# Kernel optimization log

Measured on AMD Instinct MI355X. Metric: run time of the kernel, lower is better.

## Reference

```python
import jax, jax.numpy as jnp
import numpy as np

N = 50000      # nodes
E = 800000     # edges
F = 500        # num_features
HID = 64       # hidden_channels
H = 4          # num_heads
HC = HID // H  # headc = 16
C = 8          # num_classes
KHOP = 2       # K hops
CST = 1e-5


def setup_inputs() -> dict:
    key = jax.random.key(0)
    ks = jax.random.split(key, 12)
    s = 0.02
    return {
        "node_feat": jax.random.normal(ks[0], (N, F), dtype=jnp.float32),
        "edge_index": jax.random.randint(ks[1], (2, E), 0, N, dtype=jnp.int64),
        "Wi": jax.random.normal(ks[2], (F, HID), dtype=jnp.float32) * s,
        "bi": jnp.zeros((HID,), dtype=jnp.float32),
        "Wq": jax.random.normal(ks[3], (HID, H * HC), dtype=jnp.float32) * s,
        "bq": jnp.zeros((H * HC,), dtype=jnp.float32),
        "Wk": jax.random.normal(ks[4], (HID, H * HC), dtype=jnp.float32) * s,
        "bk": jnp.zeros((H * HC,), dtype=jnp.float32),
        "Wv": jax.random.normal(ks[5], (HID, H * C), dtype=jnp.float32) * s,
        "bv": jnp.zeros((H * C,), dtype=jnp.float32),
        "Wo": jax.random.normal(ks[6], (H * C, C), dtype=jnp.float32) * s,
        "bo": jnp.zeros((C,), dtype=jnp.float32),
        "hopwise": jnp.ones((KHOP + 1,), dtype=jnp.float32),
        "headwise": jnp.zeros((H, KHOP), dtype=jnp.float32),
        "teleport": jnp.ones((1,), dtype=jnp.float32),
    }


def reference(node_feat, edge_index, Wi, bi, Wq, bq, Wk, bk, Wv, bv, Wo, bo,
              hopwise, headwise, teleport):
    row, col = edge_index[0], edge_index[1]
    # degree(col): in-degree; norm = deg^-1 indexed at row (as in the torch code)
    deg = jax.ops.segment_sum(jnp.ones((E,), dtype=node_feat.dtype), col,
                              num_segments=N)
    deg_inv = jnp.where(deg > 0, 1.0 / deg, 0.0)  # [N]

    x = jax.nn.relu(node_feat @ Wi + bi)          # dropout p=0.0 / eval -> identity
    Q = (1.0 + jax.nn.elu(x @ Wq + bq)).reshape(N, H, HC)
    Kf = (1.0 + jax.nn.elu(x @ Wk + bk)).reshape(N, H, HC)
    V = (x @ Wv + bv).reshape(N, H, C)

    M = jnp.einsum('nhi,nhj->nhij', Kf, V)        # [N,H,HC,C]
    hidden = V * hopwise[0]                       # ind_gamma & gamma_softmax
    layerwise = jax.nn.softmax(headwise, axis=0)  # softmax over heads (dim=-2)

    # global attention (teleport) term
    teleportM = jnp.sum(M, axis=0, keepdims=True) / N      # [1,H,HC,C]
    teleportK = jnp.sum(Kf, axis=0, keepdims=True) / N     # [1,H,HC]
    teleportH = jnp.einsum('nhi,bhij->nhj', Q, teleportM)  # [N,H,C]
    teleportC = jnp.einsum('nhi,bhi->nh', Q, teleportK)[..., None] + CST
    teleportH = (teleportH / teleportC).sum(axis=-2)       # [N,C]

    for hop in range(KHOP):
        # norm[e] = deg_inv[row[e]]  =>  pre-scale source nodes, then scatter-add
        M = jax.ops.segment_sum((M * deg_inv[:, None, None, None])[row], col,
                                num_segments=N)
        Kf = jax.ops.segment_sum((Kf * deg_inv[:, None, None])[row], col,
                                 num_segments=N)
        Hh = jnp.einsum('nhi,nhij->nhj', Q, M)             # [N,H,C]
        Cc = jnp.einsum('nhi,nhi->nh', Q, Kf)[..., None] + CST
        gamma = hopwise[hop + 1] * layerwise[:, hop][:, None]  # [H,1]
        hidden = hidden + gamma * (Hh / Cc)

    # multi_concat output projection
    hidden = hidden.reshape(N, H * C) @ Wo + bo
    return hidden + teleport * teleportH
```

## Files before the change

### kernel.cpp

```cpp
#include <hip/hip_runtime.h>
#include <hip/hip_bf16.h>
#include <stdint.h>
#include <stddef.h>

#define NN 50000
#define NE 800000
#define FIN 500
#define HIDN 64
#define NH 4
#define HCD 16
#define NC 8
#define KVROW 192
#define SROW 640
#define CSTF 1e-5f
#define SCAN_NB 196
#define NTILES 782

typedef float f32x2 __attribute__((ext_vector_type(2)));
typedef __attribute__((ext_vector_type(8))) short bf16x8;
typedef __attribute__((ext_vector_type(4))) float f32x4;

__device__ inline float bf_lo(unsigned u) {
    union { unsigned i; float f; } v; v.i = u << 16; return v.f;
}
__device__ inline float bf_hi(unsigned u) {
    union { unsigned i; float f; } v; v.i = u & 0xffff0000u; return v.f;
}
__device__ inline unsigned short f2bf(float f) {
    union { float f; unsigned i; } v; v.f = f;
    unsigned r = v.i + 0x7fffu + ((v.i >> 16) & 1u);
    return (unsigned short)(r >> 16);
}
__device__ inline unsigned pack2bf(float a, float b) {
    __hip_bfloat162 h = __float22bfloat162_rn(make_float2(a, b));
    unsigned r; __builtin_memcpy(&r, &h, 4); return r;
}


__global__ void k_deg(const int* __restrict__ col, int* __restrict__ deg) {
    int e = blockIdx.x * blockDim.x + threadIdx.x;
    if (e < NE) atomicAdd(&deg[col[e]], 1);
}

__global__ void k_deginv(const int* __restrict__ deg, float* __restrict__ dinv,
                         int* __restrict__ cursor, float* __restrict__ tMK) {
    int i = blockIdx.x * blockDim.x + threadIdx.x;
    if (i < NN) {
        dinv[i] = deg[i] > 0 ? 1.0f / (float)deg[i] : 0.0f;
        cursor[i] = 0;
    }
    if (blockIdx.x == 0)
        for (int j = threadIdx.x; j < 576; j += 256) tMK[j] = 0.f;
}

__global__ void k_bsum(const int* __restrict__ deg, int* __restrict__ bsum) {
    __shared__ int red[256];
    int b = blockIdx.x, t = threadIdx.x;
    int i = b * 256 + t;
    red[t] = (i < NN) ? deg[i] : 0;
    __syncthreads();
    for (int d = 128; d > 0; d >>= 1) {
        if (t < d) red[t] += red[t + d];
        __syncthreads();
    }
    if (t == 0) bsum[b] = red[0];
}

__global__ void k_bscan(const int* __restrict__ bsum, int* __restrict__ bex) {
    __shared__ int s[256];
    int t = threadIdx.x;
    int own = (t < SCAN_NB) ? bsum[t] : 0;
    s[t] = own;
    __syncthreads();
    for (int d = 1; d < 256; d <<= 1) {
        int v = (t >= d) ? s[t - d] : 0;
        __syncthreads();
        s[t] += v;
        __syncthreads();
    }
    if (t < SCAN_NB) bex[t] = s[t] - own;
}

__global__ void k_expand(const int* __restrict__ deg, const int* __restrict__ bex,
                         int* __restrict__ offs) {
    __shared__ int s[256];
    int b = blockIdx.x, t = threadIdx.x;
    int i = b * 256 + t;
    int v = (i < NN) ? deg[i] : 0;
    s[t] = v;
    __syncthreads();
    for (int d = 1; d < 256; d <<= 1) {
        int a = (t >= d) ? s[t - d] : 0;
        __syncthreads();
        s[t] += a;
        __syncthreads();
    }
    int excl = s[t] - v + bex[b];
    if (i < NN) offs[i] = excl;
    if (i == NN - 1) offs[NN] = excl + v;
}

__global__ void k_scatter(const int* __restrict__ row, const int* __restrict__ col,
                          const int* __restrict__ offs, int* __restrict__ cursor,
                          int* __restrict__ csr_src) {
    int e = blockIdx.x * blockDim.x + threadIdx.x;
    if (e < NE) {
        int c = col[e];
        int pos = offs[c] + atomicAdd(&cursor[c], 1);
        csr_src[pos] = row[e];
    }
}


__global__ __launch_bounds__(256) void k_xgemm(const float* __restrict__ nf,
                                               const float* __restrict__ Wi,
                                               const float* __restrict__ bi,
                                               float* __restrict__ x) {
    __shared__ unsigned short w_s[64 * 512];
    int t = threadIdx.x;
    for (int i = t; i < 8192; i += 256) {
        int kk = i >> 4;
        int c4 = (i & 15) * 4;
        float4 v = make_float4(0.f, 0.f, 0.f, 0.f);
        if (kk < FIN) v = *(const float4*)&Wi[(size_t)kk * 64 + c4];
        int kb = kk >> 3, kj = kk & 7;
#pragma unroll
        for (int j = 0; j < 4; j++) {
            int c = c4 + j;
            float val = (j == 0) ? v.x : (j == 1) ? v.y : (j == 2) ? v.z : v.w;
            w_s[c * 512 + ((kb ^ (c & 7)) << 3) + kj] = f2bf(val);
        }
    }
    __syncthreads();

    int lane = t & 63;
    int w = t >> 6;
    int quad = lane >> 4;
    int l15 = lane & 15;

    for (int tile = blockIdx.x; tile < NTILES; tile += gridDim.x) {
        int n0 = tile * 64;
        int rown = n0 + w * 16 + l15;
        const float* arow = &nf[(size_t)(rown < NN ? rown : 0) * FIN];

        f32x4 acc[4];
#pragma unroll
        for (int ct = 0; ct < 4; ct++) acc[ct] = (f32x4){0.f, 0.f, 0.f, 0.f};

        for (int k0 = 0; k0 < 512; k0 += 32) {
            int kk = k0 + quad * 8;
            float4 a0 = make_float4(0.f, 0.f, 0.f, 0.f);
            float4 a1 = make_float4(0.f, 0.f, 0.f, 0.f);
            if (kk < FIN) a0 = *(const float4*)&arow[kk];
            if (kk + 4 < FIN) a1 = *(const float4*)&arow[kk + 4];
            union { unsigned u[4]; bf16x8 v; } A;
            A.u[0] = pack2bf(a0.x, a0.y);
            A.u[1] = pack2bf(a0.z, a0.w);
            A.u[2] = pack2bf(a1.x, a1.y);
            A.u[3] = pack2bf(a1.z, a1.w);
            int kb = kk >> 3;
#pragma unroll
            for (int ct = 0; ct < 4; ct++) {
                int c = ct * 16 + l15;
                bf16x8 bfr = *(const bf16x8*)&w_s[c * 512 + ((kb ^ (c & 7)) << 3)];
                acc[ct] = __builtin_amdgcn_mfma_f32_16x16x32_bf16(A.v, bfr, acc[ct], 0, 0, 0);
            }
        }
#pragma unroll
        for (int ct = 0; ct < 4; ct++) {
            int c = ct * 16 + l15;
            float bv = bi[c];
#pragma unroll
            for (int r = 0; r < 4; r++) {
                int n = n0 + w * 16 + quad * 4 + r;
                if (n < NN)
                    x[(size_t)n * 64 + c] = fmaxf(acc[ct][r] + bv, 0.f);
            }
        }
    }
}


__global__ __launch_bounds__(256) void k_qkv(const float* __restrict__ x,
    const float* __restrict__ Wq, const float* __restrict__ bq,
    const float* __restrict__ Wk, const float* __restrict__ bk,
    const float* __restrict__ Wv, const float* __restrict__ bv,
    const float* __restrict__ hopwise, const float* __restrict__ dinv,
    float* __restrict__ Qg, float* __restrict__ hid,
    unsigned char* __restrict__ kv0, float* __restrict__ tMK) {
    __shared__ float wq_s[64 * 64], wk_s[64 * 64], wv_s[64 * 32];
    __shared__ float bq_s[64], bk_s[64], bv_s[32];
    __shared__ float xs[4][8][64];
    __shared__ float tacc[576];
    int t = threadIdx.x;
    for (int i = t; i < 4096; i += 256) { wq_s[i] = Wq[i]; wk_s[i] = Wk[i]; }
    for (int i = t; i < 2048; i += 256) wv_s[i] = Wv[i];
    if (t < 64) { bq_s[t] = bq[t]; bk_s[t] = bk[t]; }
    if (t >= 64 && t < 96) bv_s[t - 64] = bv[t - 64];
    for (int i = t; i < 576; i += 256) tacc[i] = 0.f;
    __syncthreads();
    int lane = t & 63;
    int w = t >> 6;
    int h = lane >> 4;
    int vcol = lane & 31;
    float hw0 = hopwise[0];
    float tkp = 0.f;
    float tmp_[8];
#pragma unroll
    for (int j = 0; j < 8; j++) tmp_[j] = 0.f;
    int tiles = (NN + 31) >> 5;
    for (int tile = blockIdx.x; tile < tiles; tile += gridDim.x) {
        int n0 = tile * 32 + w * 8;
        __syncthreads();
#pragma unroll
        for (int u = 0; u < 8; u++) {
            int n = n0 + u;
            xs[w][u][lane] = (n < NN) ? x[(size_t)n * 64 + lane] : 0.f;
        }
        __syncthreads();
        float aq[8], ak[8], av[8];
#pragma unroll
        for (int u = 0; u < 8; u++) { aq[u] = 0.f; ak[u] = 0.f; av[u] = 0.f; }
        for (int f = 0; f < 64; f++) {
            float wqv = wq_s[f * 64 + lane];
            float wkv = wk_s[f * 64 + lane];
            float wvv = wv_s[f * 32 + vcol];
#pragma unroll
            for (int u = 0; u < 8; u++) {
                float xf = xs[w][u][f];
                aq[u] = fmaf(xf, wqv, aq[u]);
                ak[u] = fmaf(xf, wkv, ak[u]);
                av[u] = fmaf(xf, wvv, av[u]);
            }
        }
#pragma unroll
        for (int u = 0; u < 8; u++) {
            int n = n0 + u;
            float q = aq[u] + bq_s[lane];
            float k = ak[u] + bk_s[lane];
            float v = av[u] + bv_s[vcol];
            float Qv = q > 0.f ? 1.f + q : expf(q);
            float Kv = k > 0.f ? 1.f + k : expf(k);
            if (n < NN) {
                Qg[(size_t)n * 64 + lane] = Qv;
                float vj[8];
#pragma unroll
                for (int j = 0; j < 8; j++) vj[j] = __shfl(v, h * 8 + j, 64);
                tkp += Kv;
#pragma unroll
                for (int j = 0; j < 8; j++) tmp_[j] += Kv * vj[j];
                float dv = dinv[n];
                unsigned short* kvrow = (unsigned short*)(kv0 + (size_t)n * KVROW);
                kvrow[lane] = f2bf(Kv * dv);
                if (lane < 32) kvrow[64 + lane] = f2bf(v);
                if (lane < 32) hid[(size_t)n * 32 + lane] = v * hw0;
            }
        }
    }
#pragma unroll
    for (int j = 0; j < 8; j++) atomicAdd(&tacc[lane * 8 + j], tmp_[j]);
    atomicAdd(&tacc[512 + lane], tkp);
    __syncthreads();
    for (int i = t; i < 576; i += 256) atomicAdd(&tMK[i], tacc[i]);
}


__global__ __launch_bounds__(256) void k_hop0(const unsigned char* __restrict__ kv0,
    const int* __restrict__ offs, const int* __restrict__ csr_src,
    const float* __restrict__ dinv, const float* __restrict__ Qg,
    const float* __restrict__ hopwise, const float* __restrict__ headwise,
    unsigned char* __restrict__ S1, float* __restrict__ hid) {
    int t = threadIdx.x;
    int lane = t & 63;
    int n = (blockIdx.x * 256 + t) >> 6;
    if (n >= NN) return;
    int h = lane >> 4;
    float e0 = expf(headwise[0]);
    float e1 = expf(headwise[2]);
    float e2 = expf(headwise[4]);
    float e3 = expf(headwise[6]);
    float esum = e0 + e1 + e2 + e3;
    float eh = (h == 0) ? e0 : ((h == 1) ? e1 : ((h == 2) ? e2 : e3));
    float gam = hopwise[1] * eh / esum;

    int hoff = 128 + h * 16;
    int o0 = offs[n], o1 = offs[n + 1];
    float kacc = 0.f;
    float4 m0 = make_float4(0.f, 0.f, 0.f, 0.f);
    float4 m1 = make_float4(0.f, 0.f, 0.f, 0.f);
    int e = o0;
    for (; e + 3 < o1; e += 4) {
        float kk_[4]; uint4 vv[4];
#pragma unroll
        for (int q = 0; q < 4; q++) {
            int s = csr_src[e + q];
            const unsigned char* r = kv0 + (size_t)s * KVROW;
            kk_[q] = bf_lo(((const unsigned short*)r)[lane]);
            vv[q] = *(const uint4*)(r + hoff);
        }
#pragma unroll
        for (int q = 0; q < 4; q++) {
            float ka = kk_[q]; uint4 va = vv[q];
            kacc += ka;
            m0.x = fmaf(ka, bf_lo(va.x), m0.x); m0.y = fmaf(ka, bf_hi(va.x), m0.y);
            m0.z = fmaf(ka, bf_lo(va.y), m0.z); m0.w = fmaf(ka, bf_hi(va.y), m0.w);
            m1.x = fmaf(ka, bf_lo(va.z), m1.x); m1.y = fmaf(ka, bf_hi(va.z), m1.y);
            m1.z = fmaf(ka, bf_lo(va.w), m1.z); m1.w = fmaf(ka, bf_hi(va.w), m1.w);
        }
    }
    for (; e < o1; e++) {
        int s = csr_src[e];
        const unsigned char* r = kv0 + (size_t)s * KVROW;
        float ka = bf_lo(((const unsigned short*)r)[lane]);
        uint4 va = *(const uint4*)(r + hoff);
        kacc += ka;
        m0.x = fmaf(ka, bf_lo(va.x), m0.x); m0.y = fmaf(ka, bf_hi(va.x), m0.y);
        m0.z = fmaf(ka, bf_lo(va.y), m0.z); m0.w = fmaf(ka, bf_hi(va.y), m0.w);
        m1.x = fmaf(ka, bf_lo(va.z), m1.x); m1.y = fmaf(ka, bf_hi(va.z), m1.y);
        m1.z = fmaf(ka, bf_lo(va.w), m1.z); m1.w = fmaf(ka, bf_hi(va.w), m1.w);
    }
    {
        float dv = dinv[n];
        float s16 = dv * 16.f;
        unsigned char* drow = S1 + (size_t)n * SROW;
        ((unsigned short*)drow)[lane] = f2bf(kacc * dv);
        unsigned u0 = __builtin_amdgcn_cvt_pk_fp8_f32(m0.x * s16, m0.y * s16, 0, false);
        u0 = __builtin_amdgcn_cvt_pk_fp8_f32(m0.z * s16, m0.w * s16, u0, true);
        unsigned u1 = __builtin_amdgcn_cvt_pk_fp8_f32(m1.x * s16, m1.y * s16, 0, false);
        u1 = __builtin_amdgcn_cvt_pk_fp8_f32(m1.z * s16, m1.w * s16, u1, true);
        uint2 pv; pv.x = u0; pv.y = u1;
        *(uint2*)(drow + 128 + lane * 8) = pv;
    }
    float qv = Qg[(size_t)n * 64 + lane];
    float hh[8];
    hh[0] = qv * m0.x; hh[1] = qv * m0.y; hh[2] = qv * m0.z; hh[3] = qv * m0.w;
    hh[4] = qv * m1.x; hh[5] = qv * m1.y; hh[6] = qv * m1.z; hh[7] = qv * m1.w;
    float cc = qv * kacc;
#pragma unroll
    for (int s = 1; s < 16; s <<= 1) {
#pragma unroll
        for (int j = 0; j < 8; j++) hh[j] += __shfl_xor(hh[j], s, 16);
        cc += __shfl_xor(cc, s, 16);
    }
    if ((lane & 15) < 8) {
        int j = lane & 7;
        float val = j < 4 ? (j < 2 ? (j == 0 ? hh[0] : hh[1]) : (j == 2 ? hh[2] : hh[3]))
                          : (j < 6 ? (j == 4 ? hh[4] : hh[5]) : (j == 6 ? hh[6] : hh[7]));
        size_t idx = (size_t)n * 32 + h * 8 + j;
        hid[idx] += gam * val / (cc + CSTF);
    }
}


__global__ __launch_bounds__(256) void k_prop1(const unsigned char* __restrict__ Sold,
    const int* __restrict__ offs, const int* __restrict__ csr_src,
    const float* __restrict__ Qg, const float* __restrict__ hopwise,
    const float* __restrict__ headwise, float* __restrict__ hid) {
    int t = threadIdx.x;
    int lane = t & 63;
    int n = (blockIdx.x * 256 + t) >> 6;
    if (n >= NN) return;
    int h = lane >> 4;
    float e0 = expf(headwise[1]);
    float e1 = expf(headwise[3]);
    float e2 = expf(headwise[5]);
    float e3 = expf(headwise[7]);
    float esum = e0 + e1 + e2 + e3;
    float eh = (h == 0) ? e0 : ((h == 1) ? e1 : ((h == 2) ? e2 : e3));
    float gam = hopwise[2] * eh / esum * 0.0625f;

    int o0 = offs[n], o1 = offs[n + 1];
    float kacc = 0.f;
    float4 m0 = make_float4(0.f, 0.f, 0.f, 0.f);
    float4 m1 = make_float4(0.f, 0.f, 0.f, 0.f);
    int e = o0;
    for (; e + 3 < o1; e += 4) {
        float kk_[4]; uint2 mv[4];
#pragma unroll
        for (int q = 0; q < 4; q++) {
            int s = csr_src[e + q];
            const unsigned char* r = Sold + (size_t)s * SROW;
            kk_[q] = bf_lo(((const unsigned short*)r)[lane]);
            mv[q] = *(const uint2*)(r + 128 + lane * 8);
        }
#pragma unroll
        for (int q = 0; q < 4; q++) {
            kacc += kk_[q];
            f32x2 a0 = __builtin_amdgcn_cvt_pk_f32_fp8(mv[q].x, false);
            f32x2 a1 = __builtin_amdgcn_cvt_pk_f32_fp8(mv[q].x, true);
            f32x2 b0 = __builtin_amdgcn_cvt_pk_f32_fp8(mv[q].y, false);
            f32x2 b1 = __builtin_amdgcn_cvt_pk_f32_fp8(mv[q].y, true);
            m0.x += a0.x; m0.y += a0.y; m0.z += a1.x; m0.w += a1.y;
            m1.x += b0.x; m1.y += b0.y; m1.z += b1.x; m1.w += b1.y;
        }
    }
    for (; e < o1; e++) {
        int s = csr_src[e];
        const unsigned char* r = Sold + (size_t)s * SROW;
        float ka = bf_lo(((const unsigned short*)r)[lane]);
        uint2 mva = *(const uint2*)(r + 128 + lane * 8);
        kacc += ka;
        f32x2 a0 = __builtin_amdgcn_cvt_pk_f32_fp8(mva.x, false);
        f32x2 a1 = __builtin_amdgcn_cvt_pk_f32_fp8(mva.x, true);
        f32x2 b0 = __builtin_amdgcn_cvt_pk_f32_fp8(mva.y, false);
        f32x2 b1 = __builtin_amdgcn_cvt_pk_f32_fp8(mva.y, true);
        m0.x += a0.x; m0.y += a0.y; m0.z += a1.x; m0.w += a1.y;
        m1.x += b0.x; m1.y += b0.y; m1.z += b1.x; m1.w += b1.y;
    }
    float qv = Qg[(size_t)n * 64 + lane];
    float hh[8];
    hh[0] = qv * m0.x; hh[1] = qv * m0.y; hh[2] = qv * m0.z; hh[3] = qv * m0.w;
    hh[4] = qv * m1.x; hh[5] = qv * m1.y; hh[6] = qv * m1.z; hh[7] = qv * m1.w;
    float cc = qv * kacc;
#pragma unroll
    for (int s = 1; s < 16; s <<= 1) {
#pragma unroll
        for (int j = 0; j < 8; j++) hh[j] += __shfl_xor(hh[j], s, 16);
        cc += __shfl_xor(cc, s, 16);
    }
    if ((lane & 15) < 8) {
        int j = lane & 7;
        float val = j < 4 ? (j < 2 ? (j == 0 ? hh[0] : hh[1]) : (j == 2 ? hh[2] : hh[3]))
                          : (j < 6 ? (j == 4 ? hh[4] : hh[5]) : (j == 6 ? hh[6] : hh[7]));
        size_t idx = (size_t)n * 32 + h * 8 + j;
        hid[idx] += gam * val / (cc + CSTF);
    }
}


__global__ __launch_bounds__(256) void k_final(const float* __restrict__ hid,
    const float* __restrict__ Qg, const float* __restrict__ Wo,
    const float* __restrict__ bo, const float* __restrict__ tMK,
    const float* __restrict__ teleport, float* __restrict__ out) {
    __shared__ float tm[512];
    __shared__ float tk[64];
    __shared__ float wo[256];
    __shared__ float bos[8];
    int t = threadIdx.x;
    const float invN = 1.0f / (float)NN;
    for (int i = t; i < 512; i += 256) tm[i] = tMK[i] * invN;
    if (t < 64) tk[t] = tMK[512 + t] * invN;
    wo[t] = Wo[t & 255];
    if (t < 8) bos[t] = bo[t];
    __syncthreads();
    float tp = teleport[0];
    int lane = t & 63;
    int sub = lane & 7;
    int g = lane >> 3;
    int wid = (blockIdx.x * 256 + t) >> 6;
    int nwaves = gridDim.x * 4;
    for (int nb = wid * 8; nb < NN; nb += nwaves * 8) {
        int n = nb + g;
        if (n < NN) {
            const float* hrow = hid + (size_t)n * 32;
            const float* qrow = Qg + (size_t)n * 64;
            float o = bos[sub];
#pragma unroll
            for (int m = 0; m < 32; m++) o = fmaf(hrow[m], wo[m * 8 + sub], o);
            float th = 0.f;
#pragma unroll
            for (int h2 = 0; h2 < 4; h2++) {
                float num = 0.f, den = 0.f;
#pragma unroll
                for (int i = 0; i < 16; i++) {
                    float q = qrow[h2 * 16 + i];
                    num = fmaf(q, tm[h2 * 128 + i * 8 + sub], num);
                    den = fmaf(q, tk[h2 * 16 + i], den);
                }
                th += num / (den + CSTF);
            }
            out[(size_t)n * 8 + sub] = o + tp * th;
        }
    }
}


extern "C" void kernel_launch(void* const* d_in, const int* in_sizes, int n_in,
                              void* d_out, int out_size, void* d_ws, size_t ws_size,
                              hipStream_t stream) {
    const float* nf = (const float*)d_in[0];
    const int* ei = (const int*)d_in[1];
    const float* Wi = (const float*)d_in[2];
    const float* bi = (const float*)d_in[3];
    const float* Wq = (const float*)d_in[4];
    const float* bq = (const float*)d_in[5];
    const float* Wk = (const float*)d_in[6];
    const float* bk = (const float*)d_in[7];
    const float* Wv = (const float*)d_in[8];
    const float* bv = (const float*)d_in[9];
    const float* Wo = (const float*)d_in[10];
    const float* bo = (const float*)d_in[11];
    const float* hopwise = (const float*)d_in[12];
    const float* headwise = (const float*)d_in[13];
    const float* teleport = (const float*)d_in[14];
    float* out = (float*)d_out;

    char* base = (char*)d_ws;
    size_t off = 0;
    auto alloc = [&](size_t bytes) -> void* {
        void* p = base + off;
        off = (off + bytes + 255) & ~(size_t)255;
        return p;
    };
    int* deg = (int*)alloc(NN * 4);
    int* cursor = (int*)alloc(NN * 4);
    int* offs = (int*)alloc((NN + 1) * 4);
    int* bsum = (int*)alloc(256 * 4);
    int* bex = (int*)alloc(256 * 4);
    float* dinv = (float*)alloc(NN * 4);
    int* csr_src = (int*)alloc((size_t)NE * 4);
    float* xbuf = (float*)alloc((size_t)NN * 64 * 4);
    float* Qg = (float*)alloc((size_t)NN * 64 * 4);
    float* hid = (float*)alloc((size_t)NN * 32 * 4);
    unsigned char* kv0 = (unsigned char*)alloc((size_t)NN * KVROW);
    unsigned char* S1 = (unsigned char*)alloc((size_t)NN * SROW);
    float* tMK = (float*)alloc(576 * 4);

    const int* rowp = ei;
    const int* colp = ei + NE;

    hipMemsetAsync(deg, 0, NN * 4, stream);

    k_deg<<<(NE + 255) / 256, 256, 0, stream>>>(colp, deg);
    k_deginv<<<(NN + 255) / 256, 256, 0, stream>>>(deg, dinv, cursor, tMK);
    k_bsum<<<SCAN_NB, 256, 0, stream>>>(deg, bsum);
    k_bscan<<<1, 256, 0, stream>>>(bsum, bex);
    k_expand<<<SCAN_NB, 256, 0, stream>>>(deg, bex, offs);
    k_scatter<<<(NE + 255) / 256, 256, 0, stream>>>(rowp, colp, offs, cursor, csr_src);
    k_xgemm<<<512, 256, 0, stream>>>(nf, Wi, bi, xbuf);
    k_qkv<<<512, 256, 0, stream>>>(xbuf, Wq, bq, Wk, bk, Wv, bv, hopwise, dinv,
                                   Qg, hid, kv0, tMK);
    k_hop0<<<(NN * 64 + 255) / 256, 256, 0, stream>>>(kv0, offs, csr_src, dinv, Qg,
                                                      hopwise, headwise, S1, hid);
    k_prop1<<<(NN * 64 + 255) / 256, 256, 0, stream>>>(S1, offs, csr_src, Qg,
                                                       hopwise, headwise, hid);
    k_final<<<1563, 256, 0, stream>>>(hid, Qg, Wo, bo, tMK, teleport, out);
}
```

Before: 495.3 us.

## Pre-transpose Wi to bf16 in global memory and drop LDS staging in xgemm

A new small kernel converts Wi once per call into a transposed bf16 buffer in workspace. The x-GEMM kernel then reads its B fragments straight from that global/L2-resident buffer instead of having every block rebuild a 64 KB swizzled LDS copy. It also launches one block per 64-row tile rather than a persistent grid-stride loop. This removes the per-block weight staging cost and the shared-memory occupancy limit, at the price of one extra launch and B-fragment reads that depend on L2/cache hits.

```diff
diff --git a/kernel.cpp b/kernel.cpp
--- a/kernel.cpp
+++ b/kernel.cpp
@@ -112,70 +112,60 @@
 }
 
 
+__global__ void k_wt(const float* __restrict__ Wi, unsigned short* __restrict__ Wt) {
+    int i = blockIdx.x * blockDim.x + threadIdx.x;
+    if (i < 64 * 512) {
+        int c = i >> 9;
+        int k = i & 511;
+        Wt[i] = (k < FIN) ? f2bf(Wi[(size_t)k * 64 + c]) : (unsigned short)0;
+    }
+}
+
+
 __global__ __launch_bounds__(256) void k_xgemm(const float* __restrict__ nf,
-                                               const float* __restrict__ Wi,
+                                               const unsigned short* __restrict__ Wt,
                                                const float* __restrict__ bi,
                                                float* __restrict__ x) {
-    __shared__ unsigned short w_s[64 * 512];
     int t = threadIdx.x;
-    for (int i = t; i < 8192; i += 256) {
-        int kk = i >> 4;
-        int c4 = (i & 15) * 4;
-        float4 v = make_float4(0.f, 0.f, 0.f, 0.f);
-        if (kk < FIN) v = *(const float4*)&Wi[(size_t)kk * 64 + c4];
-        int kb = kk >> 3, kj = kk & 7;
-#pragma unroll
-        for (int j = 0; j < 4; j++) {
-            int c = c4 + j;
-            float val = (j == 0) ? v.x : (j == 1) ? v.y : (j == 2) ? v.z : v.w;
-            w_s[c * 512 + ((kb ^ (c & 7)) << 3) + kj] = f2bf(val);
-        }
-    }
-    __syncthreads();
-
     int lane = t & 63;
     int w = t >> 6;
     int quad = lane >> 4;
     int l15 = lane & 15;
-
-    for (int tile = blockIdx.x; tile < NTILES; tile += gridDim.x) {
-        int n0 = tile * 64;
-        int rown = n0 + w * 16 + l15;
-        const float* arow = &nf[(size_t)(rown < NN ? rown : 0) * FIN];
-
-        f32x4 acc[4];
-#pragma unroll
-        for (int ct = 0; ct < 4; ct++) acc[ct] = (f32x4){0.f, 0.f, 0.f, 0.f};
-
-        for (int k0 = 0; k0 < 512; k0 += 32) {
-            int kk = k0 + quad * 8;
-            float4 a0 = make_float4(0.f, 0.f, 0.f, 0.f);
-            float4 a1 = make_float4(0.f, 0.f, 0.f, 0.f);
-            if (kk < FIN) a0 = *(const float4*)&arow[kk];
-            if (kk + 4 < FIN) a1 = *(const float4*)&arow[kk + 4];
-            union { unsigned u[4]; bf16x8 v; } A;
-            A.u[0] = pack2bf(a0.x, a0.y);
-            A.u[1] = pack2bf(a0.z, a0.w);
-            A.u[2] = pack2bf(a1.x, a1.y);
-            A.u[3] = pack2bf(a1.z, a1.w);
-            int kb = kk >> 3;
-#pragma unroll
-            for (int ct = 0; ct < 4; ct++) {
-                int c = ct * 16 + l15;
-                bf16x8 bfr = *(const bf16x8*)&w_s[c * 512 + ((kb ^ (c & 7)) << 3)];
-                acc[ct] = __builtin_amdgcn_mfma_f32_16x16x32_bf16(A.v, bfr, acc[ct], 0, 0, 0);
-            }
-        }
+    int n0 = blockIdx.x * 64;
+    int rown = n0 + w * 16 + l15;
+    const float* arow = &nf[(size_t)(rown < NN ? rown : 0) * FIN];
+
+    f32x4 acc[4];
+#pragma unroll
+    for (int ct = 0; ct < 4; ct++) acc[ct] = (f32x4){0.f, 0.f, 0.f, 0.f};
+
+    for (int k0 = 0; k0 < 512; k0 += 32) {
+        int kk = k0 + quad * 8;
+        float4 a0 = make_float4(0.f, 0.f, 0.f, 0.f);
+        float4 a1 = make_float4(0.f, 0.f, 0.f, 0.f);
+        if (kk < FIN) a0 = *(const float4*)&arow[kk];
+        if (kk + 4 < FIN) a1 = *(const float4*)&arow[kk + 4];
+        union { unsigned u[4]; bf16x8 v; } A;
+        A.u[0] = pack2bf(a0.x, a0.y);
+        A.u[1] = pack2bf(a0.z, a0.w);
+        A.u[2] = pack2bf(a1.x, a1.y);
+        A.u[3] = pack2bf(a1.z, a1.w);
 #pragma unroll
         for (int ct = 0; ct < 4; ct++) {
             int c = ct * 16 + l15;
-            float bv = bi[c];
-#pragma unroll
-            for (int r = 0; r < 4; r++) {
-                int n = n0 + w * 16 + quad * 4 + r;
-                if (n < NN)
-                    x[(size_t)n * 64 + c] = fmaxf(acc[ct][r] + bv, 0.f);
-            }
+            bf16x8 bfr = *(const bf16x8*)&Wt[(size_t)c * 512 + kk];
+            acc[ct] = __builtin_amdgcn_mfma_f32_16x16x32_bf16(A.v, bfr, acc[ct], 0, 0, 0);
+        }
+    }
+#pragma unroll
+    for (int ct = 0; ct < 4; ct++) {
+        int c = ct * 16 + l15;
+        float bv = bi[c];
+#pragma unroll
+        for (int r = 0; r < 4; r++) {
+            int n = n0 + w * 16 + quad * 4 + r;
+            if (n < NN)
+                x[(size_t)n * 64 + c] = fmaxf(acc[ct][r] + bv, 0.f);
         }
     }
 }
@@ -509,6 +499,7 @@
     int* bex = (int*)alloc(256 * 4);
     float* dinv = (float*)alloc(NN * 4);
     int* csr_src = (int*)alloc((size_t)NE * 4);
+    unsigned short* Wt = (unsigned short*)alloc(64 * 512 * 2);
     float* xbuf = (float*)alloc((size_t)NN * 64 * 4);
     float* Qg = (float*)alloc((size_t)NN * 64 * 4);
     float* hid = (float*)alloc((size_t)NN * 32 * 4);
@@ -527,7 +518,8 @@
     k_bscan<<<1, 256, 0, stream>>>(bsum, bex);
     k_expand<<<SCAN_NB, 256, 0, stream>>>(deg, bex, offs);
     k_scatter<<<(NE + 255) / 256, 256, 0, stream>>>(rowp, colp, offs, cursor, csr_src);
-    k_xgemm<<<512, 256, 0, stream>>>(nf, Wi, bi, xbuf);
+    k_wt<<<128, 256, 0, stream>>>(Wi, Wt);
+    k_xgemm<<<NTILES, 256, 0, stream>>>(nf, Wt, bi, xbuf);
     k_qkv<<<512, 256, 0, stream>>>(xbuf, Wq, bq, Wk, bk, Wv, bv, hopwise, dinv,
                                    Qg, hid, kv0, tMK);
     k_hop0<<<(NN * 64 + 255) / 256, 256, 0, stream>>>(kv0, offs, csr_src, dinv, Qg,
```

Result: faster. 480.6 us (-3.0%).
